# Performance work log

Measured on AMD Instinct MI355X. Metric: run time of the kernel, lower is better.

The kernel has to match this reference:

```python
import jax
import jax.numpy as jnp
import numpy as np

TOKENS, D_IN, D_OUT = 8192, 4096, 4096
QMAX = 127.0


def setup_inputs() -> dict:
    key = jax.random.key(0)
    k_x, k_w, k_s, k_o, k_b = jax.random.split(key, 5)
    x = jax.random.normal(k_x, (TOKENS, D_IN), dtype=jnp.float32)
    # int8-valued weight stored as int32 for portability (values in [-127, 127])
    weight = jax.random.randint(k_w, (D_OUT, D_IN), -127, 128, dtype=jnp.int32)
    # realistic small per-channel dequant scales
    weight_scale = (jax.random.uniform(k_s, (D_OUT,), dtype=jnp.float32) + 0.5) * 0.01
    # module stores -weight_offset; keep small integer-ish zero points
    weight_offset = jnp.round(jax.random.normal(k_o, (D_OUT,), dtype=jnp.float32) * 4.0)
    bias = jax.random.normal(k_b, (D_OUT,), dtype=jnp.float32) * 0.1
    return {"x": x, "weight": weight, "weight_scale": weight_scale,
            "weight_offset": weight_offset, "bias": bias}


def reference(x, weight, weight_scale, weight_offset, bias):
    # --- dynamic per-token symmetric activation quantization ---
    act_scale = jnp.max(jnp.abs(x), axis=-1, keepdims=True) / QMAX   # [T, 1]
    x_q = jnp.clip(jnp.round(x / act_scale), -QMAX, QMAX)            # int-valued fp32 [T, D_in]

    # --- int8 GEMM with per-channel zero-point correction ---
    # stored weight_offset = -zero_point, so dequant weight = scale * (w_q + weight_offset)
    acc = x_q @ weight.astype(jnp.float32).T                          # [T, D_out]
    zp_corr = jnp.sum(x_q, axis=-1, keepdims=True) * weight_offset[None, :]
    acc = acc + zp_corr

    # --- dequant + bias epilogue ---
    y = acc * act_scale * weight_scale[None, :] + bias[None, :]
    return y
```

## Files before the change

### kernel.cpp

```cpp
#include <hip/hip_runtime.h>
#include <cstdint>
#include <cstddef>

#define TOKENS 8192
#define DIN    4096
#define DOUT   4096

typedef int int4v __attribute__((ext_vector_type(4)));

__global__ __launch_bounds__(256) void quant_rows(const float* __restrict__ x,
                                                  int* __restrict__ xq,
                                                  float* __restrict__ ascale,
                                                  int* __restrict__ rsum) {
  const int row = blockIdx.x;
  const int t = threadIdx.x;
  const float4* xr = (const float4*)(x + (size_t)row * DIN);
  float4 v[4];
#pragma unroll
  for (int i = 0; i < 4; ++i) v[i] = xr[i * 256 + t];

  float m = 0.f;
#pragma unroll
  for (int i = 0; i < 4; ++i) {
    m = fmaxf(m, fabsf(v[i].x)); m = fmaxf(m, fabsf(v[i].y));
    m = fmaxf(m, fabsf(v[i].z)); m = fmaxf(m, fabsf(v[i].w));
  }
#pragma unroll
  for (int off = 32; off; off >>= 1) m = fmaxf(m, __shfl_xor(m, off));

  __shared__ float wmax[4];
  __shared__ int   wsum[4];
  const int lane = t & 63, wid = t >> 6;
  if (lane == 0) wmax[wid] = m;
  __syncthreads();
  m = fmaxf(fmaxf(wmax[0], wmax[1]), fmaxf(wmax[2], wmax[3]));

  const float s = m * (1.0f / 127.0f);
  const float sdiv = (m > 0.f) ? s : 1.0f;

  int ssum = 0;
#pragma unroll
  for (int i = 0; i < 4; ++i) {
    float q;
    q = fminf(fmaxf(rintf(v[i].x / sdiv), -127.f), 127.f); const int b0 = (int)q;
    q = fminf(fmaxf(rintf(v[i].y / sdiv), -127.f), 127.f); const int b1 = (int)q;
    q = fminf(fmaxf(rintf(v[i].z / sdiv), -127.f), 127.f); const int b2 = (int)q;
    q = fminf(fmaxf(rintf(v[i].w / sdiv), -127.f), 127.f); const int b3 = (int)q;
    ssum += b0 + b1 + b2 + b3;
    xq[(size_t)row * 1024 + i * 256 + t] =
        (b0 & 255) | ((b1 & 255) << 8) | ((b2 & 255) << 16) | ((b3 & 255) << 24);
  }
#pragma unroll
  for (int off = 32; off; off >>= 1) ssum += __shfl_xor(ssum, off);
  if (lane == 0) wsum[wid] = ssum;
  __syncthreads();
  if (t == 0) {
    rsum[row]   = wsum[0] + wsum[1] + wsum[2] + wsum[3];
    ascale[row] = s;
  }
}

__global__ __launch_bounds__(256) void wconv(const int* __restrict__ w,
                                             int* __restrict__ w8) {
  const int idx = blockIdx.x * 256 + threadIdx.x;
  const int4 v = ((const int4*)w)[idx];
  w8[idx] = (v.x & 255) | ((v.y & 255) << 8) | ((v.z & 255) << 16) | ((v.w & 255) << 24);
}

__device__ __forceinline__ void gload_lds16(const char* g, char* l) {
  __builtin_amdgcn_global_load_lds(
      (const __attribute__((address_space(1))) void*)g,
      (__attribute__((address_space(3))) void*)l, 16, 0, 0);
}

#define MFMA_QUAD(MB)                                                         \
  _Pragma("unroll")                                                           \
  for (int m = 0; m < 4; ++m)                                                 \
    _Pragma("unroll")                                                         \
    for (int n = 0; n < 4; ++n)                                               \
      acc[m + MB][n] = __builtin_amdgcn_mfma_i32_16x16x64_i8(                 \
          a[m], bf[n], acc[m + MB][n], 0, 0, 0);

#define TILE_STEP(T_, DOSTAGE_, VMN_)                                         \
  do {                                                                        \
    const char* Lb = lds + ((T_) & 3) * 32768;                                \
    char* Wb = lds + (((T_) + 3) & 3) * 32768;                                \
    const size_t ko = (size_t)((T_) + 3) * 64;                                \
    int4v a[4], bf[4];                                                        \
    _Pragma("unroll")                                                         \
    for (int m = 0; m < 4; ++m)                                               \
      a[m] = *(const int4v*)(Lb + aoff + m * 1024);                           \
    _Pragma("unroll")                                                         \
    for (int n = 0; n < 4; ++n)                                               \
      bf[n] = *(const int4v*)(Lb + boff + n * 1024);                          \
    if (DOSTAGE_) {                                                           \
      gload_lds16(gA0 + ko, Wb + ldst);                                       \
      gload_lds16(gA1 + ko, Wb + 8192 + ldst);                                \
    }                                                                         \
    __builtin_amdgcn_s_barrier();                                             \
    __builtin_amdgcn_s_setprio(1);                                            \
    __builtin_amdgcn_sched_barrier(0);                                        \
    MFMA_QUAD(0)                                                              \
    __builtin_amdgcn_s_setprio(0);                                            \
    __builtin_amdgcn_s_barrier();                                             \
    _Pragma("unroll")                                                         \
    for (int m = 0; m < 4; ++m)                                               \
      a[m] = *(const int4v*)(Lb + aoff + (m + 4) * 1024);                     \
    if (DOSTAGE_) {                                                           \
      gload_lds16(gB0 + ko, Wb + 16384 + ldst);                               \
      gload_lds16(gB1 + ko, Wb + 24576 + ldst);                               \
    }                                                                         \
    __builtin_amdgcn_s_barrier();                                             \
    __builtin_amdgcn_s_setprio(1);                                            \
    __builtin_amdgcn_sched_barrier(0);                                        \
    MFMA_QUAD(4)                                                              \
    __builtin_amdgcn_s_setprio(0);                                            \
    if ((VMN_) == 8)      asm volatile("s_waitcnt vmcnt(8)" ::: "memory");    \
    else if ((VMN_) == 4) asm volatile("s_waitcnt vmcnt(4)" ::: "memory");    \
    else if ((VMN_) == 0) asm volatile("s_waitcnt vmcnt(0)" ::: "memory");    \
    __builtin_amdgcn_s_barrier();                                             \
  } while (0)

__global__ __launch_bounds__(512, 2) void gemm_i8(
    const char* __restrict__ xq, const char* __restrict__ w8,
    const float* __restrict__ ascale, const int* __restrict__ rsum,
    const float* __restrict__ wscale, const float* __restrict__ woff,
    const float* __restrict__ bias, float* __restrict__ y) {

  __shared__ __align__(16) char lds[131072];

  const int bid = blockIdx.x;
  const int tm = bid >> 4;
  const int tn = bid & 15;
  const int t = threadIdx.x;
  const int lane = t & 63, wid = t >> 6;
  const int wmI = wid >> 2;
  const int wnI = wid & 3;

  const int srow = t >> 2;
  const int scol = ((t & 3) ^ ((t >> 3) & 3)) * 16;

  const char* gA0 = xq + (size_t)(tm * 256 + srow) * DIN + scol;
  const char* gA1 = gA0 + (size_t)128 * DIN;
  const char* gB0 = w8 + (size_t)(tn * 256 + srow) * DIN + scol;
  const char* gB1 = gB0 + (size_t)128 * DIN;
  const int ldst = t * 16;

  const int frow = lane & 15;
  const int swz  = ((lane >> 4) * 16) ^ (((frow >> 1) & 3) << 4);
  const int aoff = wmI * 8192 + frow * 64 + swz;
  const int boff = (2 + (wnI >> 1)) * 8192 + (wnI & 1) * 4096 + frow * 64 + swz;

  int4v acc[8][4];
#pragma unroll
  for (int m = 0; m < 8; ++m)
#pragma unroll
    for (int n = 0; n < 4; ++n) acc[m][n] = (int4v){0, 0, 0, 0};

#pragma unroll
  for (int p = 0; p < 3; ++p) {
    char* Wb = lds + p * 32768;
    gload_lds16(gA0 + p * 64, Wb + ldst);
    gload_lds16(gA1 + p * 64, Wb + 8192 + ldst);
    gload_lds16(gB0 + p * 64, Wb + 16384 + ldst);
    gload_lds16(gB1 + p * 64, Wb + 24576 + ldst);
  }
  asm volatile("s_waitcnt vmcnt(8)" ::: "memory");
  __builtin_amdgcn_s_barrier();

  for (int T = 0; T < 61; ++T) TILE_STEP(T, true, 8);
  TILE_STEP(61, false, 4);
  TILE_STEP(62, false, 0);
  TILE_STEP(63, false, -1);

  const int rb0 = tm * 256 + wmI * 128 + (lane >> 4) * 4;
  const int cb0 = tn * 256 + wnI * 64 + (lane & 15);
#pragma unroll
  for (int n = 0; n < 4; ++n) {
    const int col = cb0 + n * 16;
    const float ws_ = wscale[col];
    const float wo_ = woff[col];
    const float bi_ = bias[col];
#pragma unroll
    for (int m = 0; m < 8; ++m) {
      const int r0 = rb0 + m * 16;
#pragma unroll
      for (int j = 0; j < 4; ++j) {
        const int r = r0 + j;
        const float acf = (float)acc[m][n][j] + (float)rsum[r] * wo_;
        y[(size_t)r * DOUT + col] = acf * (ascale[r] * ws_) + bi_;
      }
    }
  }
}

extern "C" void kernel_launch(void* const* d_in, const int* in_sizes, int n_in,
                              void* d_out, int out_size, void* d_ws, size_t ws_size,
                              hipStream_t stream) {
  const float* x      = (const float*)d_in[0];
  const int*   w      = (const int*)  d_in[1];
  const float* wscale = (const float*)d_in[2];
  const float* woff   = (const float*)d_in[3];
  const float* bias   = (const float*)d_in[4];
  float* y = (float*)d_out;

  char* ws = (char*)d_ws;
  char*  xq     = ws;
  char*  w8     = ws + (size_t)TOKENS * DIN;
  float* ascale = (float*)(w8 + (size_t)DOUT * DIN);
  int*   rsum   = (int*)(ascale + TOKENS);

  hipLaunchKernelGGL(quant_rows, dim3(TOKENS), dim3(256), 0, stream,
                     x, (int*)xq, ascale, rsum);
  hipLaunchKernelGGL(wconv, dim3((DOUT * DIN / 4) / 256), dim3(256), 0, stream,
                     w, (int*)w8);
  hipLaunchKernelGGL(gemm_i8, dim3((TOKENS / 256) * (DOUT / 256)), dim3(512), 0, stream,
                     xq, w8, ascale, rsum, wscale, woff, bias, y);
}
```

Before: 242.4 us.

## Switch GEMM to 32x32x32 int8 MFMA with register double-buffered LDS fragments

```diff
diff --git a/kernel.cpp b/kernel.cpp
--- a/kernel.cpp
+++ b/kernel.cpp
@@ -6,7 +6,8 @@
 #define DIN    4096
 #define DOUT   4096
 
-typedef int int4v __attribute__((ext_vector_type(4)));
+typedef int int4v  __attribute__((ext_vector_type(4)));
+typedef int int16v __attribute__((ext_vector_type(16)));
 
 __global__ __launch_bounds__(256) void quant_rows(const float* __restrict__ x,
                                                   int* __restrict__ xq,
@@ -73,52 +74,51 @@
       (__attribute__((address_space(3))) void*)l, 16, 0, 0);
 }
 
-#define MFMA_QUAD(MB)                                                         \
+#define MFMA8(AV, BV)                                                         \
+  __builtin_amdgcn_s_setprio(1);                                              \
   _Pragma("unroll")                                                           \
-  for (int m = 0; m < 4; ++m)                                                 \
+  for (int mi = 0; mi < 4; ++mi)                                              \
     _Pragma("unroll")                                                         \
-    for (int n = 0; n < 4; ++n)                                               \
-      acc[m + MB][n] = __builtin_amdgcn_mfma_i32_16x16x64_i8(                 \
-          a[m], bf[n], acc[m + MB][n], 0, 0, 0);
-
-#define TILE_STEP(T_, DOSTAGE_, VMN_)                                         \
+    for (int ni = 0; ni < 2; ++ni)                                            \
+      acc[mi][ni] = __builtin_amdgcn_mfma_i32_32x32x32_i8(                    \
+          AV[mi], BV[ni], acc[mi][ni], 0, 0, 0);                              \
+  __builtin_amdgcn_s_setprio(0);
+
+#define TILE_BODY(T_, STAGE_, VMN_, NEXT_)                                    \
   do {                                                                        \
     const char* Lb = lds + ((T_) & 3) * 32768;                                \
     char* Wb = lds + (((T_) + 3) & 3) * 32768;                                \
-    const size_t ko = (size_t)((T_) + 3) * 64;                                \
-    int4v a[4], bf[4];                                                        \
-    _Pragma("unroll")                                                         \
-    for (int m = 0; m < 4; ++m)                                               \
-      a[m] = *(const int4v*)(Lb + aoff + m * 1024);                           \
-    _Pragma("unroll")                                                         \
-    for (int n = 0; n < 4; ++n)                                               \
-      bf[n] = *(const int4v*)(Lb + boff + n * 1024);                          \
-    if (DOSTAGE_) {                                                           \
+    if (STAGE_) {                                                             \
+      const size_t ko = (size_t)((T_) + 3) * 64;                              \
       gload_lds16(gA0 + ko, Wb + ldst);                                       \
       gload_lds16(gA1 + ko, Wb + 8192 + ldst);                                \
-    }                                                                         \
-    __builtin_amdgcn_s_barrier();                                             \
-    __builtin_amdgcn_s_setprio(1);                                            \
-    __builtin_amdgcn_sched_barrier(0);                                        \
-    MFMA_QUAD(0)                                                              \
-    __builtin_amdgcn_s_setprio(0);                                            \
-    __builtin_amdgcn_s_barrier();                                             \
-    _Pragma("unroll")                                                         \
-    for (int m = 0; m < 4; ++m)                                               \
-      a[m] = *(const int4v*)(Lb + aoff + (m + 4) * 1024);                     \
-    if (DOSTAGE_) {                                                           \
       gload_lds16(gB0 + ko, Wb + 16384 + ldst);                               \
       gload_lds16(gB1 + ko, Wb + 24576 + ldst);                               \
     }                                                                         \
-    __builtin_amdgcn_s_barrier();                                             \
-    __builtin_amdgcn_s_setprio(1);                                            \
-    __builtin_amdgcn_sched_barrier(0);                                        \
-    MFMA_QUAD(4)                                                              \
-    __builtin_amdgcn_s_setprio(0);                                            \
-    if ((VMN_) == 8)      asm volatile("s_waitcnt vmcnt(8)" ::: "memory");    \
-    else if ((VMN_) == 4) asm volatile("s_waitcnt vmcnt(4)" ::: "memory");    \
-    else if ((VMN_) == 0) asm volatile("s_waitcnt vmcnt(0)" ::: "memory");    \
-    __builtin_amdgcn_s_barrier();                                             \
+    _Pragma("unroll")                                                         \
+    for (int mi = 0; mi < 4; ++mi)                                            \
+      aB[mi] = *(const int4v*)(Lb + aoff1 + mi * 2048);                       \
+    _Pragma("unroll")                                                         \
+    for (int ni = 0; ni < 2; ++ni)                                            \
+      bB[ni] = *(const int4v*)(Lb + boff1 + ni * 2048);                       \
+    MFMA8(aA, bA)                                                             \
+    if ((VMN_) >= 0) {                                                        \
+      if ((VMN_) == 8)      asm volatile("s_waitcnt vmcnt(8)" ::: "memory");  \
+      else if ((VMN_) == 4) asm volatile("s_waitcnt vmcnt(4)" ::: "memory");  \
+      else                  asm volatile("s_waitcnt vmcnt(0)" ::: "memory");  \
+      asm volatile("s_waitcnt lgkmcnt(0)" ::: "memory");                      \
+      __builtin_amdgcn_s_barrier();                                           \
+    }                                                                         \
+    if (NEXT_) {                                                              \
+      const char* Ln = lds + (((T_) + 1) & 3) * 32768;                        \
+      _Pragma("unroll")                                                       \
+      for (int mi = 0; mi < 4; ++mi)                                          \
+        aA[mi] = *(const int4v*)(Ln + aoff0 + mi * 2048);                     \
+      _Pragma("unroll")                                                       \
+      for (int ni = 0; ni < 2; ++ni)                                          \
+        bA[ni] = *(const int4v*)(Ln + boff0 + ni * 2048);                     \
+    }                                                                         \
+    MFMA8(aB, bB)                                                             \
   } while (0)
 
 __global__ __launch_bounds__(512, 2) void gemm_i8(
@@ -146,16 +146,23 @@
   const char* gB1 = gB0 + (size_t)128 * DIN;
   const int ldst = t * 16;
 
-  const int frow = lane & 15;
-  const int swz  = ((lane >> 4) * 16) ^ (((frow >> 1) & 3) << 4);
-  const int aoff = wmI * 8192 + frow * 64 + swz;
-  const int boff = (2 + (wnI >> 1)) * 8192 + (wnI & 1) * 4096 + frow * 64 + swz;
-
-  int4v acc[8][4];
-#pragma unroll
-  for (int m = 0; m < 8; ++m)
-#pragma unroll
-    for (int n = 0; n < 4; ++n) acc[m][n] = (int4v){0, 0, 0, 0};
+  const int mask  = ((lane >> 1) & 3) << 4;
+  const int chunk = (lane >> 5) * 16;
+  const int aoff0 = wmI * 8192 + (lane & 31) * 64 + ((chunk +  0) ^ mask);
+  const int aoff1 = wmI * 8192 + (lane & 31) * 64 + ((chunk + 32) ^ mask);
+  const int bbase = (2 + (wnI >> 1)) * 8192 + (wnI & 1) * 4096 + (lane & 31) * 64;
+  const int boff0 = bbase + ((chunk +  0) ^ mask);
+  const int boff1 = bbase + ((chunk + 32) ^ mask);
+
+  int16v acc[4][2];
+#pragma unroll
+  for (int mi = 0; mi < 4; ++mi)
+#pragma unroll
+    for (int ni = 0; ni < 2; ++ni)
+#pragma unroll
+      for (int rg = 0; rg < 16; ++rg) acc[mi][ni][rg] = 0;
+
+  int4v aA[4], bA[2], aB[4], bB[2];
 
 #pragma unroll
   for (int p = 0; p < 3; ++p) {
@@ -167,29 +174,30 @@
   }
   asm volatile("s_waitcnt vmcnt(8)" ::: "memory");
   __builtin_amdgcn_s_barrier();
-
-  for (int T = 0; T < 61; ++T) TILE_STEP(T, true, 8);
-  TILE_STEP(61, false, 4);
-  TILE_STEP(62, false, 0);
-  TILE_STEP(63, false, -1);
-
-  const int rb0 = tm * 256 + wmI * 128 + (lane >> 4) * 4;
-  const int cb0 = tn * 256 + wnI * 64 + (lane & 15);
-#pragma unroll
-  for (int n = 0; n < 4; ++n) {
-    const int col = cb0 + n * 16;
-    const float ws_ = wscale[col];
-    const float wo_ = woff[col];
-    const float bi_ = bias[col];
-#pragma unroll
-    for (int m = 0; m < 8; ++m) {
-      const int r0 = rb0 + m * 16;
-#pragma unroll
-      for (int j = 0; j < 4; ++j) {
-        const int r = r0 + j;
-        const float acf = (float)acc[m][n][j] + (float)rsum[r] * wo_;
-        y[(size_t)r * DOUT + col] = acf * (ascale[r] * ws_) + bi_;
-      }
+#pragma unroll
+  for (int mi = 0; mi < 4; ++mi) aA[mi] = *(const int4v*)(lds + aoff0 + mi * 2048);
+#pragma unroll
+  for (int ni = 0; ni < 2; ++ni) bA[ni] = *(const int4v*)(lds + boff0 + ni * 2048);
+
+  for (int T = 0; T < 61; ++T) TILE_BODY(T, 1, 8, 1);
+  TILE_BODY(61, 0, 4, 1);
+  TILE_BODY(62, 0, 0, 1);
+  TILE_BODY(63, 0, -1, 0);
+
+  const int rb0 = tm * 256 + wmI * 128 + 4 * (lane >> 5);
+  const int cb0 = tn * 256 + wnI * 64 + (lane & 31);
+  const float ws0 = wscale[cb0],      ws1 = wscale[cb0 + 32];
+  const float wo0 = woff[cb0],        wo1 = woff[cb0 + 32];
+  const float bi0 = bias[cb0],        bi1 = bias[cb0 + 32];
+#pragma unroll
+  for (int mi = 0; mi < 4; ++mi) {
+#pragma unroll
+    for (int rg = 0; rg < 16; ++rg) {
+      const int r = rb0 + mi * 32 + (rg & 3) + 8 * (rg >> 2);
+      const float as_ = ascale[r];
+      const float rs_ = (float)rsum[r];
+      y[(size_t)r * DOUT + cb0]      = ((float)acc[mi][0][rg] + rs_ * wo0) * (as_ * ws0) + bi0;
+      y[(size_t)r * DOUT + cb0 + 32] = ((float)acc[mi][1][rg] + rs_ * wo1) * (as_ * ws1) + bi1;
     }
   }
 }
```

Result: faster. 198.3 us (-18.2%).
